# Performance work log

Hardware: AMD Instinct MI355X
Metric: run time of the kernel (lower is better)

Reference implementation:

```python
import jax, jax.numpy as jnp
import numpy as np
from jax import lax

EPS = 1e-12  # F.normalize default eps


def setup_inputs() -> dict:
    key = jax.random.key(0)
    ks = jax.random.split(key, 4)
    b, dim, h, w = 8, 192, 128, 128
    num_heads = 6
    x = jax.random.normal(ks[0], (b, dim, h, w), dtype=jnp.float32)
    y = jax.random.normal(ks[1], (b, dim, h, w), dtype=jnp.float32)
    # depthwise conv weight (groups = 3*dim): [3*dim, 1, 3, 3]
    w_dw = jax.random.normal(ks[2], (3 * dim, 1, 3, 3), dtype=jnp.float32) * 0.1
    # 1x1 projection: [dim, dim]
    w_proj = jax.random.normal(ks[3], (dim, dim), dtype=jnp.float32) * (1.0 / np.sqrt(dim))
    temperature = jnp.ones((num_heads, 1, 1), dtype=jnp.float32)
    return {"x": x, "y": y, "w_dw": w_dw, "w_proj": w_proj,
            "temperature": temperature, "num_heads": num_heads}


def _l2norm(t):
    n = jnp.sqrt(jnp.sum(t * t, axis=-1, keepdims=True))
    return t / jnp.maximum(n, EPS)


def reference(x, y, w_dw, w_proj, temperature, num_heads):
    b, c, h, w = x.shape
    qkv_in = jnp.concatenate([x, y, y], axis=1)  # [b, 3c, h, w]
    # depthwise 3x3 conv, stride 1, padding 1 (groups = 3c)
    qkv = lax.conv_general_dilated(
        qkv_in, w_dw, window_strides=(1, 1), padding=((1, 1), (1, 1)),
        dimension_numbers=("NCHW", "OIHW", "NCHW"), feature_group_count=3 * c)
    q, k, v = jnp.split(qkv, 3, axis=1)
    ch = c // num_heads
    rs = lambda t: t.reshape(b, num_heads, ch, h * w)  # b head c (h w)
    q, k, v = rs(q), rs(k), rs(v)
    q = _l2norm(q)
    k = _l2norm(k)
    # channel attention: [b, head, ch, ch]
    attn = jnp.einsum("bhcn,bhdn->bhcd", q, k) * temperature
    attn = jax.nn.softmax(attn, axis=-1)
    out = jnp.einsum("bhcd,bhdn->bhcn", attn, v).reshape(b, c, h, w)
    # 1x1 conv projection
    out = jnp.einsum("oc,bchw->bohw", w_proj, out)
    return out
```

## Files before the change

kernel.cpp:

```cpp
#include <hip/hip_runtime.h>
#include <hip/hip_bf16.h>

#define DEV __device__ __forceinline__

typedef unsigned short u16;
typedef unsigned int u32;
typedef __attribute__((ext_vector_type(8))) short short8;
typedef __attribute__((ext_vector_type(4))) float f32x4;

DEV u16 f2bf(float f) {
  __hip_bfloat16 h = __float2bfloat16(f);
  return *(u16*)&h;
}
DEV float bf2f_s(short s) { return __uint_as_float(((u32)(u16)s) << 16); }

#define NB 8
#define NH 6
#define CTOT 192
#define HW 16384
#define VTS 34
#define LSTR 136

__global__ __launch_bounds__(256) void kconv(
    const float* __restrict__ x, const float* __restrict__ y,
    const float* __restrict__ wdw,
    u16* __restrict__ qws, u16* __restrict__ kws, u16* __restrict__ vws)
{
  __shared__ __align__(16) float lds[66 * LSTR];
  const int t = threadIdx.x, lane = t & 63, w = t >> 6;
  const int bx   = blockIdx.x;
  const int iskv = bx & 1;
  const int rest = bx >> 1;
  const int chp  = rest & 1;
  const int task = rest >> 1;
  const int b  = task / 192;
  const int gc = task % 192;
  const int r0 = chp * 64;

  const float* __restrict__ in =
      (iskv ? y : x) + (((size_t)(b * CTOT + gc)) << 14);

  float w0[9], w1[9];
  if (!iskv) {
#pragma unroll
    for (int i = 0; i < 9; ++i) w0[i] = wdw[gc * 9 + i];
  } else {
#pragma unroll
    for (int i = 0; i < 9; ++i) {
      w0[i] = wdw[(CTOT + gc) * 9 + i];
      w1[i] = wdw[(2 * CTOT + gc) * 9 + i];
    }
  }

  if (t < 132) {
    const int row = t >> 1;
    lds[row * LSTR + ((t & 1) ? 132 : 3)] = 0.f;
  }
#pragma unroll
  for (int i = 0; i < 9; ++i) {
    const int idx = i * 256 + t;
    if (idx < 2112) {
      const int row = idx >> 5, c4 = idx & 31;
      const int grow = r0 - 1 + row;
      float4 v = (grow >= 0 && grow < 128)
          ? *(const float4*)(in + grow * 128 + c4 * 4)
          : make_float4(0.f, 0.f, 0.f, 0.f);
      *(float4*)&lds[row * LSTR + 4 + c4 * 4] = v;
    }
  }
  __syncthreads();

  const int j    = lane & 31;
  const int half = lane >> 5;
  u16* __restrict__ out0 =
      (iskv ? kws : qws) + (((size_t)(b * CTOT + gc)) << 14);
  u16* __restrict__ out1 = vws + (((size_t)(b * CTOT + gc)) << 14);

#pragma unroll
  for (int i = 0; i < 8; ++i) {
    const int lrow = w * 16 + i * 2 + half;
    const int r = r0 + lrow;

    float  lt[3], rt[3];
    float4 md[3];
#pragma unroll
    for (int dr = 0; dr < 3; ++dr) {
      const int base = (lrow + dr) * LSTR + 4 * j;
      lt[dr] = lds[base + 3];
      md[dr] = *(const float4*)&lds[base + 4];
      rt[dr] = lds[base + 8];
    }

    {
      float o0 = 0.f, o1 = 0.f, o2 = 0.f, o3 = 0.f;
#pragma unroll
      for (int dr = 0; dr < 3; ++dr) {
        const float a = lt[dr], b0 = md[dr].x, c = md[dr].y,
                    d = md[dr].z, e = md[dr].w, f = rt[dr];
        o0 = fmaf(w0[dr * 3 + 0], a,  o0); o0 = fmaf(w0[dr * 3 + 1], b0, o0); o0 = fmaf(w0[dr * 3 + 2], c, o0);
        o1 = fmaf(w0[dr * 3 + 0], b0, o1); o1 = fmaf(w0[dr * 3 + 1], c,  o1); o1 = fmaf(w0[dr * 3 + 2], d, o1);
        o2 = fmaf(w0[dr * 3 + 0], c,  o2); o2 = fmaf(w0[dr * 3 + 1], d,  o2); o2 = fmaf(w0[dr * 3 + 2], e, o2);
        o3 = fmaf(w0[dr * 3 + 0], d,  o3); o3 = fmaf(w0[dr * 3 + 1], e,  o3); o3 = fmaf(w0[dr * 3 + 2], f, o3);
      }
      const u32 p01 = ((u32)f2bf(o1) << 16) | (u32)f2bf(o0);
      const u32 p23 = ((u32)f2bf(o3) << 16) | (u32)f2bf(o2);
      *(uint2*)(out0 + r * 128 + 4 * j) = make_uint2(p01, p23);
    }
    if (iskv) {
      float o0 = 0.f, o1 = 0.f, o2 = 0.f, o3 = 0.f;
#pragma unroll
      for (int dr = 0; dr < 3; ++dr) {
        const float a = lt[dr], b0 = md[dr].x, c = md[dr].y,
                    d = md[dr].z, e = md[dr].w, f = rt[dr];
        o0 = fmaf(w1[dr * 3 + 0], a,  o0); o0 = fmaf(w1[dr * 3 + 1], b0, o0); o0 = fmaf(w1[dr * 3 + 2], c, o0);
        o1 = fmaf(w1[dr * 3 + 0], b0, o1); o1 = fmaf(w1[dr * 3 + 1], c,  o1); o1 = fmaf(w1[dr * 3 + 2], d, o1);
        o2 = fmaf(w1[dr * 3 + 0], c,  o2); o2 = fmaf(w1[dr * 3 + 1], d,  o2); o2 = fmaf(w1[dr * 3 + 2], e, o2);
        o3 = fmaf(w1[dr * 3 + 0], d,  o3); o3 = fmaf(w1[dr * 3 + 1], e,  o3); o3 = fmaf(w1[dr * 3 + 2], f, o3);
      }
      const u32 p01 = ((u32)f2bf(o1) << 16) | (u32)f2bf(o0);
      const u32 p23 = ((u32)f2bf(o3) << 16) | (u32)f2bf(o2);
      *(uint2*)(out1 + r * 128 + 4 * j) = make_uint2(p01, p23);
    }
  }
}

__global__ __launch_bounds__(256) void k2a_gram(
    const u16* __restrict__ qws, const u16* __restrict__ kws,
    float* __restrict__ gram, float* __restrict__ sqq, float* __restrict__ sqk)
{
  const int t = threadIdx.x, l = t & 63, w = t >> 6;
  const int bh = blockIdx.x >> 4, tile = blockIdx.x & 15;
  const int p0 = tile * 1024 + w * 256;
  const u16* qb = qws + (((size_t)bh) << 19);
  const u16* kb = kws + (((size_t)bh) << 19);
  const int row = l & 15;
  const int kq  = (l >> 4) * 8;

  f32x4 acc[2][2] = {};
  float sq[2] = {0.f, 0.f}, sk[2] = {0.f, 0.f};

  for (int ks = 0; ks < 8; ++ks) {
    const int p = p0 + ks * 32 + kq;
    short8 av[2], bv[2];
#pragma unroll
    for (int tc = 0; tc < 2; ++tc) {
      av[tc] = *(const short8*)(qb + (((size_t)(tc * 16 + row)) << 14) + p);
      bv[tc] = *(const short8*)(kb + (((size_t)(tc * 16 + row)) << 14) + p);
    }
#pragma unroll
    for (int tc = 0; tc < 2; ++tc) {
#pragma unroll
      for (int j = 0; j < 8; ++j) {
        float fa = bf2f_s(av[tc][j]); sq[tc] = fmaf(fa, fa, sq[tc]);
        float fb = bf2f_s(bv[tc][j]); sk[tc] = fmaf(fb, fb, sk[tc]);
      }
    }
#pragma unroll
    for (int tc = 0; tc < 2; ++tc)
#pragma unroll
      for (int td = 0; td < 2; ++td)
        acc[tc][td] = __builtin_amdgcn_mfma_f32_16x16x32_bf16(av[tc], bv[td], acc[tc][td], 0, 0, 0);
  }

#pragma unroll
  for (int tc = 0; tc < 2; ++tc)
#pragma unroll
    for (int td = 0; td < 2; ++td)
#pragma unroll
      for (int rr = 0; rr < 4; ++rr) {
        int c = tc * 16 + (l >> 4) * 4 + rr;
        int d = td * 16 + row;
        atomicAdd(gram + (size_t)bh * 1024 + c * 32 + d, acc[tc][td][rr]);
      }

#pragma unroll
  for (int tc = 0; tc < 2; ++tc) {
    sq[tc] += __shfl_xor(sq[tc], 16);
    sq[tc] += __shfl_xor(sq[tc], 32);
    sk[tc] += __shfl_xor(sk[tc], 16);
    sk[tc] += __shfl_xor(sk[tc], 32);
  }
  if ((l >> 4) == 0) {
#pragma unroll
    for (int tc = 0; tc < 2; ++tc) {
      atomicAdd(sqq + bh * 32 + tc * 16 + row, sq[tc]);
      atomicAdd(sqk + bh * 32 + tc * 16 + row, sk[tc]);
    }
  }
}

__global__ __launch_bounds__(256) void k2b_w2(
    const float* __restrict__ gram, const float* __restrict__ sqq,
    const float* __restrict__ sqk, const float* __restrict__ wp,
    const float* __restrict__ temp, u16* __restrict__ W2)
{
  __shared__ float Ls[32][33];
  __shared__ float As[32][33];
  __shared__ float wl[192 * 32];
  __shared__ float nq[32], nk[32];
  const int t = threadIdx.x;
  const int bh = blockIdx.x, b = bh / 6, h = bh % 6;
  const float tmp = temp[h];
  if (t < 32) nq[t] = fmaxf(sqrtf(sqq[bh * 32 + t]), 1e-12f);
  else if (t < 64) nk[t - 32] = fmaxf(sqrtf(sqk[bh * 32 + t - 32]), 1e-12f);
  __syncthreads();
#pragma unroll
  for (int i = 0; i < 4; ++i) {
    int idx = i * 256 + t, c = idx >> 5, d = idx & 31;
    Ls[c][d] = gram[(size_t)bh * 1024 + idx] / (nq[c] * nk[d]) * tmp;
  }
  __syncthreads();
  if (t < 32) {
    float m = -1e30f;
#pragma unroll
    for (int d = 0; d < 32; ++d) m = fmaxf(m, Ls[t][d]);
    float s = 0.f;
#pragma unroll
    for (int d = 0; d < 32; ++d) s += expf(Ls[t][d] - m);
    float inv = 1.0f / s;
#pragma unroll
    for (int d = 0; d < 32; ++d) As[t][d] = expf(Ls[t][d] - m) * inv;
  }
  for (int i = 0; i < 24; ++i) {
    int idx = i * 256 + t, o = idx >> 5, c = idx & 31;
    wl[idx] = wp[o * 192 + h * 32 + c];
  }
  __syncthreads();
  for (int i = 0; i < 24; ++i) {
    int idx = i * 256 + t, o = idx >> 5, d = idx & 31;
    float a = 0.f;
#pragma unroll
    for (int c = 0; c < 32; ++c) a = fmaf(wl[o * 32 + c], As[c][d], a);
    W2[((size_t)(b * 192 + o)) * 192 + h * 32 + d] = f2bf(a);
  }
}

__global__ __launch_bounds__(256) void k3_gemm(
    const u16* __restrict__ W2, const u16* __restrict__ vnat,
    float* __restrict__ out)
{
  __shared__ __align__(16) u16 b_tile[128 * VTS];
  __shared__ __align__(16) float cout[32 * 132];
  const int t = threadIdx.x, l = t & 63, w = t >> 6;
  const int bx = blockIdx.x;
  const int b  = bx >> 7, nb = bx & 127;
  const int arow = l & 15;
  const int kq8  = (l >> 4) * 8;
  const u16* w2b = W2 + (size_t)b * 192 * 192;
  const u16* vb  = vnat + ((size_t)b * CTOT) * HW;
  const int n0 = nb * 128;

  f32x4 acc[12][2] = {};

  for (int ks = 0; ks < 6; ++ks) {
    if (ks > 0) __syncthreads();
#pragma unroll
    for (int r2 = 0; r2 < 2; ++r2) {
      const int ch   = (t >> 4) + r2 * 16;
      const int nseg = (t & 15) * 8;
      short8 vv = *(const short8*)(vb + (size_t)(ks * 32 + ch) * HW + n0 + nseg);
#pragma unroll
      for (int j = 0; j < 8; ++j) b_tile[(nseg + j) * VTS + ch] = (u16)vv[j];
    }
    __syncthreads();

    short8 bf[2];
#pragma unroll
    for (int nt = 0; nt < 2; ++nt)
      bf[nt] = *(const short8*)&b_tile[(w * 32 + nt * 16 + arow) * VTS + kq8];
#pragma unroll
    for (int ot = 0; ot < 12; ++ot) {
      short8 af = *(const short8*)(w2b + (size_t)(ot * 16 + arow) * 192 + ks * 32 + kq8);
#pragma unroll
      for (int nt = 0; nt < 2; ++nt)
        acc[ot][nt] = __builtin_amdgcn_mfma_f32_16x16x32_bf16(af, bf[nt], acc[ot][nt], 0, 0, 0);
    }
  }

  float* __restrict__ ob = out + ((size_t)b * 192) * 16384;
#pragma unroll
  for (int og = 0; og < 6; ++og) {
    __syncthreads();
#pragma unroll
    for (int oi = 0; oi < 2; ++oi) {
#pragma unroll
      for (int nt = 0; nt < 2; ++nt)
#pragma unroll
        for (int rr = 0; rr < 4; ++rr) {
          const int o_l = oi * 16 + (l >> 4) * 4 + rr;
          const int n_l = w * 32 + nt * 16 + (l & 15);
          cout[o_l * 132 + n_l] = acc[og * 2 + oi][nt][rr];
        }
    }
    __syncthreads();
    const int o_l = t >> 3;
    const int o   = og * 32 + o_l;
#pragma unroll
    for (int c = 0; c < 4; ++c) {
      const int n = (t & 7) * 4 + c * 32;
      float4 v4;
      v4.x = cout[o_l * 132 + n + 0];
      v4.y = cout[o_l * 132 + n + 1];
      v4.z = cout[o_l * 132 + n + 2];
      v4.w = cout[o_l * 132 + n + 3];
      *(float4*)(ob + (size_t)o * 16384 + n0 + n) = v4;
    }
  }
}

extern "C" void kernel_launch(void* const* d_in, const int* in_sizes, int n_in,
                              void* d_out, int out_size, void* d_ws, size_t ws_size,
                              hipStream_t stream)
{
  const float* x    = (const float*)d_in[0];
  const float* y    = (const float*)d_in[1];
  const float* wdw  = (const float*)d_in[2];
  const float* wp   = (const float*)d_in[3];
  const float* temp = (const float*)d_in[4];

  char* ws = (char*)d_ws;
  const size_t QK = (size_t)NB * CTOT * HW * 2;
  u16*   qws  = (u16*)(ws);
  u16*   kws  = (u16*)(ws + QK);
  u16*   vws  = (u16*)(ws + 2 * QK);
  float* gram = (float*)(ws + 3 * QK);
  float* sqq  = (float*)(ws + 3 * QK + 196608);
  float* sqk  = (float*)(ws + 3 * QK + 196608 + 6144);
  u16*   W2   = (u16*)(ws + 3 * QK + 196608 + 12288);
  float* out  = (float*)d_out;

  hipMemsetAsync(ws + 3 * QK, 0, 208896, stream);
  kconv<<<6144, 256, 0, stream>>>(x, y, wdw, qws, kws, vws);
  k2a_gram<<<768, 256, 0, stream>>>(qws, kws, gram, sqq, sqk);
  k2b_w2<<<48, 256, 0, stream>>>(gram, sqq, sqk, wp, temp, W2);
  k3_gemm<<<1024, 256, 0, stream>>>(W2, vws, out);
}
```

Baseline: 174.4 us.

## Store Q/K as FP8 and move squared-norm reduction into conv kernel

The depthwise conv now writes Q and K as packed FP8 instead of bf16, and the gram kernel uses the FP8 MFMA on them. The L2 norm sums are now computed in fp32 inside the conv kernel and accumulated with one atomic per block, so the gram kernel no longer converts and squares elements. This halves Q/K write and read traffic and removes ALU work from the gram pass, at the cost of lower precision in the Q·K dot products and the default-scaled FP8 range.

```diff
diff --git a/kernel.cpp b/kernel.cpp
--- a/kernel.cpp
+++ b/kernel.cpp
@@ -3,8 +3,10 @@
 
 #define DEV __device__ __forceinline__
 
+typedef unsigned char u8;
 typedef unsigned short u16;
 typedef unsigned int u32;
+typedef long long i64;
 typedef __attribute__((ext_vector_type(8))) short short8;
 typedef __attribute__((ext_vector_type(4))) float f32x4;
 
@@ -12,7 +14,6 @@
   __hip_bfloat16 h = __float2bfloat16(f);
   return *(u16*)&h;
 }
-DEV float bf2f_s(short s) { return __uint_as_float(((u32)(u16)s) << 16); }
 
 #define NB 8
 #define NH 6
@@ -24,7 +25,8 @@
 __global__ __launch_bounds__(256) void kconv(
     const float* __restrict__ x, const float* __restrict__ y,
     const float* __restrict__ wdw,
-    u16* __restrict__ qws, u16* __restrict__ kws, u16* __restrict__ vws)
+    u8* __restrict__ qws, u8* __restrict__ kws, u16* __restrict__ vws,
+    float* __restrict__ sqq, float* __restrict__ sqk)
 {
   __shared__ __align__(16) float lds[66 * LSTR];
   const int t = threadIdx.x, lane = t & 63, w = t >> 6;
@@ -72,9 +74,11 @@
 
   const int j    = lane & 31;
   const int half = lane >> 5;
-  u16* __restrict__ out0 =
+  u8*  __restrict__ out0 =
       (iskv ? kws : qws) + (((size_t)(b * CTOT + gc)) << 14);
   u16* __restrict__ out1 = vws + (((size_t)(b * CTOT + gc)) << 14);
+
+  float ssum = 0.f;
 
 #pragma unroll
   for (int i = 0; i < 8; ++i) {
@@ -102,9 +106,11 @@
         o2 = fmaf(w0[dr * 3 + 0], c,  o2); o2 = fmaf(w0[dr * 3 + 1], d,  o2); o2 = fmaf(w0[dr * 3 + 2], e, o2);
         o3 = fmaf(w0[dr * 3 + 0], d,  o3); o3 = fmaf(w0[dr * 3 + 1], e,  o3); o3 = fmaf(w0[dr * 3 + 2], f, o3);
       }
-      const u32 p01 = ((u32)f2bf(o1) << 16) | (u32)f2bf(o0);
-      const u32 p23 = ((u32)f2bf(o3) << 16) | (u32)f2bf(o2);
-      *(uint2*)(out0 + r * 128 + 4 * j) = make_uint2(p01, p23);
+      ssum = fmaf(o0, o0, ssum); ssum = fmaf(o1, o1, ssum);
+      ssum = fmaf(o2, o2, ssum); ssum = fmaf(o3, o3, ssum);
+      u32 p = (u32)__builtin_amdgcn_cvt_pk_fp8_f32(o0, o1, 0, false);
+      p = (u32)__builtin_amdgcn_cvt_pk_fp8_f32(o2, o3, (int)p, true);
+      *(u32*)(out0 + r * 128 + 4 * j) = p;
     }
     if (iskv) {
       float o0 = 0.f, o1 = 0.f, o2 = 0.f, o3 = 0.f;
@@ -122,44 +128,44 @@
       *(uint2*)(out1 + r * 128 + 4 * j) = make_uint2(p01, p23);
     }
   }
+
+  ssum += __shfl_xor(ssum, 1);
+  ssum += __shfl_xor(ssum, 2);
+  ssum += __shfl_xor(ssum, 4);
+  ssum += __shfl_xor(ssum, 8);
+  ssum += __shfl_xor(ssum, 16);
+  ssum += __shfl_xor(ssum, 32);
+  if (lane == 0)
+    atomicAdd((iskv ? sqk : sqq) + b * CTOT + gc, ssum);
 }
 
 __global__ __launch_bounds__(256) void k2a_gram(
-    const u16* __restrict__ qws, const u16* __restrict__ kws,
-    float* __restrict__ gram, float* __restrict__ sqq, float* __restrict__ sqk)
+    const u8* __restrict__ qws, const u8* __restrict__ kws,
+    float* __restrict__ gram)
 {
   const int t = threadIdx.x, l = t & 63, w = t >> 6;
   const int bh = blockIdx.x >> 4, tile = blockIdx.x & 15;
   const int p0 = tile * 1024 + w * 256;
-  const u16* qb = qws + (((size_t)bh) << 19);
-  const u16* kb = kws + (((size_t)bh) << 19);
+  const u8* qb = qws + (((size_t)bh) << 19);
+  const u8* kb = kws + (((size_t)bh) << 19);
   const int row = l & 15;
   const int kq  = (l >> 4) * 8;
 
   f32x4 acc[2][2] = {};
-  float sq[2] = {0.f, 0.f}, sk[2] = {0.f, 0.f};
 
   for (int ks = 0; ks < 8; ++ks) {
     const int p = p0 + ks * 32 + kq;
-    short8 av[2], bv[2];
+    i64 av[2], bv[2];
 #pragma unroll
     for (int tc = 0; tc < 2; ++tc) {
-      av[tc] = *(const short8*)(qb + (((size_t)(tc * 16 + row)) << 14) + p);
-      bv[tc] = *(const short8*)(kb + (((size_t)(tc * 16 + row)) << 14) + p);
-    }
-#pragma unroll
-    for (int tc = 0; tc < 2; ++tc) {
-#pragma unroll
-      for (int j = 0; j < 8; ++j) {
-        float fa = bf2f_s(av[tc][j]); sq[tc] = fmaf(fa, fa, sq[tc]);
-        float fb = bf2f_s(bv[tc][j]); sk[tc] = fmaf(fb, fb, sk[tc]);
-      }
+      av[tc] = *(const i64*)(qb + (((size_t)(tc * 16 + row)) << 14) + p);
+      bv[tc] = *(const i64*)(kb + (((size_t)(tc * 16 + row)) << 14) + p);
     }
 #pragma unroll
     for (int tc = 0; tc < 2; ++tc)
 #pragma unroll
       for (int td = 0; td < 2; ++td)
-        acc[tc][td] = __builtin_amdgcn_mfma_f32_16x16x32_bf16(av[tc], bv[td], acc[tc][td], 0, 0, 0);
+        acc[tc][td] = __builtin_amdgcn_mfma_f32_16x16x32_fp8_fp8(av[tc], bv[td], acc[tc][td], 0, 0, 0);
   }
 
 #pragma unroll
@@ -172,21 +178,6 @@
         int d = td * 16 + row;
         atomicAdd(gram + (size_t)bh * 1024 + c * 32 + d, acc[tc][td][rr]);
       }
-
-#pragma unroll
-  for (int tc = 0; tc < 2; ++tc) {
-    sq[tc] += __shfl_xor(sq[tc], 16);
-    sq[tc] += __shfl_xor(sq[tc], 32);
-    sk[tc] += __shfl_xor(sk[tc], 16);
-    sk[tc] += __shfl_xor(sk[tc], 32);
-  }
-  if ((l >> 4) == 0) {
-#pragma unroll
-    for (int tc = 0; tc < 2; ++tc) {
-      atomicAdd(sqq + bh * 32 + tc * 16 + row, sq[tc]);
-      atomicAdd(sqk + bh * 32 + tc * 16 + row, sk[tc]);
-    }
-  }
 }
 
 __global__ __launch_bounds__(256) void k2b_w2(
@@ -319,19 +310,21 @@
   const float* temp = (const float*)d_in[4];
 
   char* ws = (char*)d_ws;
-  const size_t QK = (size_t)NB * CTOT * HW * 2;
-  u16*   qws  = (u16*)(ws);
-  u16*   kws  = (u16*)(ws + QK);
-  u16*   vws  = (u16*)(ws + 2 * QK);
-  float* gram = (float*)(ws + 3 * QK);
-  float* sqq  = (float*)(ws + 3 * QK + 196608);
-  float* sqk  = (float*)(ws + 3 * QK + 196608 + 6144);
-  u16*   W2   = (u16*)(ws + 3 * QK + 196608 + 12288);
+  const size_t QK8 = (size_t)NB * CTOT * HW;
+  const size_t VBF = (size_t)NB * CTOT * HW * 2;
+  u8*    qws  = (u8*)(ws);
+  u8*    kws  = (u8*)(ws + QK8);
+  u16*   vws  = (u16*)(ws + 2 * QK8);
+  char*  meta = ws + 2 * QK8 + VBF;
+  float* gram = (float*)(meta);
+  float* sqq  = (float*)(meta + 196608);
+  float* sqk  = (float*)(meta + 196608 + 6144);
+  u16*   W2   = (u16*)(meta + 196608 + 12288);
   float* out  = (float*)d_out;
 
-  hipMemsetAsync(ws + 3 * QK, 0, 208896, stream);
-  kconv<<<6144, 256, 0, stream>>>(x, y, wdw, qws, kws, vws);
-  k2a_gram<<<768, 256, 0, stream>>>(qws, kws, gram, sqq, sqk);
+  hipMemsetAsync(meta, 0, 208896, stream);
+  kconv<<<6144, 256, 0, stream>>>(x, y, wdw, qws, kws, vws, sqq, sqk);
+  k2a_gram<<<768, 256, 0, stream>>>(qws, kws, gram);
   k2b_w2<<<48, 256, 0, stream>>>(gram, sqq, sqk, wp, temp, W2);
   k3_gemm<<<1024, 256, 0, stream>>>(W2, vws, out);
 }
```

Measured after the change: 172.1 us. Within noise of the previous version (-1.3%).
